# Kernel optimization log

Hardware: AMD Instinct MI355X
Metric: run time of the kernel (lower is better)

The kernel has to match this reference:

```python
import jax, jax.numpy as jnp
import numpy as np

MAX_DET = 300   # max_det in non_max_suppression
IMG = 640       # input image H=W
MH = MW = 160   # proto mask resolution
NM = 32         # mask coefficients
ALPHA = 0.6
MARGIN = 15


def setup_inputs() -> dict:
    key = jax.random.key(0)
    k1, k2, k3, k4, k5, k6 = jax.random.split(key, 6)
    na = 8400
    # realistic YOLOv8 raw head output: xywh in pixels, 1 class score in (0,1), 32 mask coeffs
    cxcy = jax.random.uniform(k1, (1, 2, na), minval=0.0, maxval=float(IMG))
    wh = jax.random.uniform(k2, (1, 2, na), minval=10.0, maxval=200.0)
    cls = jax.random.uniform(k3, (1, 1, na))
    mcoef = jax.random.normal(k4, (1, NM, na))
    prediction = jnp.concatenate([cxcy, wh, cls, mcoef], axis=1)  # [1,37,8400]
    proto = jax.random.normal(k5, (1, NM, MH, MW))
    img = jax.random.uniform(k6, (1, 3, IMG, IMG))
    return {"prediction": prediction, "proto": proto, "img": img,
            "conf_thres": jnp.float32(0.25), "iou_thres": jnp.float32(0.45)}


def _xywh2xyxy(x):
    cx, cy, w, h = x[..., 0], x[..., 1], x[..., 2], x[..., 3]
    return jnp.stack([cx - w / 2, cy - h / 2, cx + w / 2, cy + h / 2], axis=-1)


def _box_iou(b):  # b: [K,4] xyxy -> [K,K] pairwise IoU (torchvision convention)
    x1, y1, x2, y2 = b[:, 0], b[:, 1], b[:, 2], b[:, 3]
    area = (x2 - x1) * (y2 - y1)
    iw = jnp.clip(jnp.minimum(x2[:, None], x2[None, :]) - jnp.maximum(x1[:, None], x1[None, :]), 0)
    ih = jnp.clip(jnp.minimum(y2[:, None], y2[None, :]) - jnp.maximum(y1[:, None], y1[None, :]), 0)
    inter = iw * ih
    return inter / (area[:, None] + area[None, :] - inter + 1e-7)


def _nms_keep(iou, valid, iou_thres):
    # sequential greedy suppression over score-sorted boxes (padded, fixed K)
    K = iou.shape[0]
    def body(keep, i):
        suppressed = jnp.any(keep & (iou[i] > iou_thres))
        keep = keep.at[i].set(valid[i] & ~suppressed)
        return keep, None
    keep, _ = jax.lax.scan(body, jnp.zeros((K,), bool), jnp.arange(K))
    return keep


def reference(prediction, proto, img, conf_thres, iou_thres):
    # --- decode: [1,37,na] -> [na,37], xywh->xyxy (bs=1, nc=1, class offset c = 0*max_wh = 0)
    p = prediction[0].T                      # [na,37]
    boxes = _xywh2xyxy(p[:, :4])             # [na,4]
    conf = p[:, 4]                           # nc=1 -> max over classes is the class itself, j=0
    mcoef = p[:, 5:]                         # [na,32]
    valid = conf > conf_thres
    score = jnp.where(valid, conf, -1.0)
    order = jnp.argsort(-score)[:MAX_DET]    # top max_det candidates by confidence
    boxes_k, score_k, m_k = boxes[order], score[order], mcoef[order]
    valid_k = valid[order]
    # --- NMS (padded)
    keep = _nms_keep(_box_iou(boxes_k), valid_k, iou_thres)  # [K] bool
    # --- process_mask: linear combine protos, sigmoid, crop, bilinear upsample, >0.5
    masks = jax.nn.sigmoid(m_k @ proto[0].reshape(NM, -1)).reshape(MAX_DET, MH, MW)
    scale = jnp.array([MW / IMG, MH / IMG, MW / IMG, MH / IMG], dtype=boxes_k.dtype)
    db = boxes_k * scale                     # downsampled bboxes [K,4]
    r = jnp.arange(MW, dtype=masks.dtype)[None, None, :]
    c = jnp.arange(MH, dtype=masks.dtype)[None, :, None]
    crop = ((r >= db[:, 0, None, None]) & (r < db[:, 2, None, None]) &
            (c >= db[:, 1, None, None]) & (c < db[:, 3, None, None]))
    masks = masks * crop
    masks_up = jax.image.resize(masks, (MAX_DET, IMG, IMG), method='linear')  # align_corners=False bilinear
    masks_bin = (masks_up > 0.5) & keep[:, None, None]       # invalid/suppressed rows zeroed
    # --- scale_boxes: img1_shape == img0_shape -> gain=1, pad=0, just clip
    boxes_c = jnp.clip(boxes_k, 0.0, float(IMG))
    results = jnp.concatenate([boxes_c, score_k[:, None], jnp.zeros((MAX_DET, 1), boxes_c.dtype)], axis=1)
    results = results * keep[:, None].astype(results.dtype)  # [K,6] padded detections
    # --- max-area box -> crop window coords
    areas = jnp.where(keep, (boxes_c[:, 2] - boxes_c[:, 0]) * (boxes_c[:, 3] - boxes_c[:, 1]), 0.0)
    mb = jnp.where(jnp.any(keep), boxes_c[jnp.argmax(areas)], jnp.zeros(4, boxes_c.dtype))
    y1 = jnp.maximum(mb[1].astype(jnp.int32) - MARGIN, 0)
    y2 = jnp.minimum(mb[3].astype(jnp.int32) + MARGIN, IMG)
    x1 = jnp.maximum(mb[0].astype(jnp.int32) - MARGIN, 0)
    x2 = jnp.minimum(mb[2].astype(jnp.int32) + MARGIN, IMG)
    crop_coords = jnp.stack([y1, y2, x1, x2])
    # --- mask overlay blending (stack over images, sum over detections)
    stacked_mk = jnp.sum(masks_bin.astype(img.dtype), axis=0)[None]  # [1,640,640]
    pixels = jnp.count_nonzero(stacked_mk)
    blue = jnp.zeros((3, IMG, IMG), img.dtype).at[2].set(1.0)
    img_out = (1.0 - stacked_mk) * img + stacked_mk * (ALPHA * img + (1.0 - ALPHA) * blue)
    return results, keep, masks_bin, pixels, img_out, crop_coords
```

## Files before the change

### kernel.cpp

```cpp
#include <hip/hip_runtime.h>
#include <stdint.h>

#define NA 8400
#define MAXD 300
#define NMC 32
#define IMGD 640
#define MH 160
#define MW 160
#define PROTO_HW (MH*MW)
#define IMG_HW (IMGD*IMGD)

#define OFF_RESULTS 0
#define OFF_KEEP    1800
#define OFF_MASKS   2100
#define OFF_PIXELS  (2100 + 300*IMG_HW)
#define OFF_IMG     (OFF_PIXELS + 1)
#define OFF_CROP    (OFF_IMG + 3*IMG_HW)

#define WSO_MASKS160 0
#define WSO_KEYS     (MAXD*PROTO_HW*4)
#define WSO_HIST     (WSO_KEYS + NA*8)
#define WSO_META     (WSO_HIST + 1024*4)
#define WSO_ORDER    (WSO_META + 64)
#define WSO_VFLAG    (WSO_ORDER + MAXD*4)
#define WSO_SCORE    (WSO_VFLAG + MAXD*4)
#define WSO_BOXES    (WSO_SCORE + MAXD*4)
#define WSO_MCOEF    (WSO_BOXES + MAXD*16)
#define WSO_KEEPI    (WSO_MCOEF + MAXD*NMC*4)
#define WSO_KLIST    (WSO_KEEPI + MAXD*4)
#define WSO_EBOX     (WSO_KLIST + MAXD*4)

#define NSB 33
#define NFILL 30000

__global__ __launch_bounds__(256)
void k_score_fill(const float* __restrict__ pred, const float* __restrict__ conf_thres_p,
                  uint64_t* __restrict__ keys, unsigned* __restrict__ hist,
                  float* __restrict__ out_masks) {
    int bid = blockIdx.x;
    if (bid >= NSB) {
        size_t f = (size_t)(bid - NSB) * 4096 + (size_t)threadIdx.x * 16;
        float4 z = {0.f, 0.f, 0.f, 0.f};
        float4* p = (float4*)(out_masks + f);
        p[0] = z; p[1] = z; p[2] = z; p[3] = z;
        return;
    }
    int i = bid * 256 + threadIdx.x;
    if (i >= NA) return;
    float th = *conf_thres_p;
    float conf = pred[4 * NA + i];
    uint64_t key = 0;
    if (conf > th) {
        unsigned fb = __float_as_uint(conf);
        key = ((uint64_t)fb << 32) | (unsigned)(NA - 1 - i);
        int bin = (int)(conf * 1024.0f);
        bin = bin < 0 ? 0 : (bin > 1023 ? 1023 : bin);
        atomicAdd(&hist[bin], 1u);
    }
    keys[i] = key;
}

__global__ __launch_bounds__(1024)
void k_select(const float* __restrict__ pred, const uint64_t* __restrict__ keys,
              const unsigned* __restrict__ hist,
              int* __restrict__ vflag, float* __restrict__ score_k,
              float* __restrict__ boxes_k, float* __restrict__ mcoef_k) {
    __shared__ unsigned cum[1024];
    __shared__ uint64_t kl[2048];
    __shared__ uint64_t srt[MAXD];
    __shared__ int s_cnt, s_bcut, s_nsel;
    __shared__ int sorder[MAXD];
    __shared__ int svf[MAXD];
    int t = threadIdx.x;

    cum[t] = hist[t];
    __syncthreads();
    for (int off = 1; off < 1024; off <<= 1) {
        unsigned v = cum[t] + ((t + off < 1024) ? cum[t + off] : 0u);
        __syncthreads();
        cum[t] = v;
        __syncthreads();
    }
    if (t == 0) {
        s_cnt = 0;
        int tot = (int)cum[0];
        s_nsel = tot < MAXD ? tot : MAXD;
        s_bcut = 0;
    }
    __syncthreads();
    int nsel = s_nsel;
    if (nsel > 0) {
        if (cum[t] >= (unsigned)nsel && (t == 1023 || cum[t + 1] < (unsigned)nsel))
            s_bcut = t;
    }
    __syncthreads();
    int bcut = s_bcut;
    if (nsel > 0) {
        for (int i = t; i < NA; i += 1024) {
            uint64_t key = keys[i];
            if (key) {
                float conf = __uint_as_float((unsigned)(key >> 32));
                int bin = (int)(conf * 1024.0f);
                bin = bin > 1023 ? 1023 : bin;
                if (bin >= bcut) {
                    int p = atomicAdd(&s_cnt, 1);
                    if (p < 2048) kl[p] = key;
                }
            }
        }
    }
    __syncthreads();
    int cnt = s_cnt < 2048 ? s_cnt : 2048;
    for (int c = t; c < cnt; c += 1024) {
        uint64_t key = kl[c];
        int rank = 0;
        for (int j = 0; j < cnt; j++) rank += (kl[j] > key) ? 1 : 0;
        if (rank < MAXD) srt[rank] = key;
    }
    __syncthreads();
    if (t < MAXD) {
        int v = (t < nsel) ? 1 : 0;
        uint64_t key = v ? srt[t] : 0;
        int idx = v ? (NA - 1 - (int)(key & 0xffffffffu)) : 0;
        sorder[t] = idx; svf[t] = v;
        vflag[t] = v;
        score_k[t] = v ? __uint_as_float((unsigned)(key >> 32)) : -1.0f;
        float cx = pred[0 * NA + idx], cy = pred[1 * NA + idx];
        float w = pred[2 * NA + idx], h = pred[3 * NA + idx];
        float b0 = cx - w * 0.5f, b1 = cy - h * 0.5f, b2 = cx + w * 0.5f, b3 = cy + h * 0.5f;
        if (!v) { b0 = b1 = b2 = b3 = 0.f; }
        boxes_k[t * 4 + 0] = b0; boxes_k[t * 4 + 1] = b1;
        boxes_k[t * 4 + 2] = b2; boxes_k[t * 4 + 3] = b3;
    }
    __syncthreads();
    for (int m = t; m < MAXD * NMC; m += 1024) {
        int r = m >> 5, c = m & 31;
        mcoef_k[m] = svf[r] ? pred[(5 + c) * NA + sorder[r]] : 0.f;
    }
}

__global__ __launch_bounds__(512)
void k_nms(const float* __restrict__ iou_thres_p, const int* __restrict__ vflag,
           const float* __restrict__ boxes_k, const float* __restrict__ score_k,
           int* __restrict__ keepi, int* __restrict__ klist, int* __restrict__ meta,
           int* __restrict__ ebox, float* __restrict__ out) {
    __shared__ uint64_t su[MAXD][5];
    __shared__ float bx[MAXD][4];
    __shared__ float sarea[MAXD];
    __shared__ int sv[MAXD];
    __shared__ int skeep[MAXD];
    int t = threadIdx.x;
    for (int i = t; i < MAXD; i += 512) {
        float b0 = boxes_k[i * 4 + 0], b1 = boxes_k[i * 4 + 1];
        float b2 = boxes_k[i * 4 + 2], b3 = boxes_k[i * 4 + 3];
        bx[i][0] = b0; bx[i][1] = b1; bx[i][2] = b2; bx[i][3] = b3;
        sarea[i] = (b2 - b0) * (b3 - b1);
        sv[i] = vflag[i];
    }
    __syncthreads();
    float ithr = *iou_thres_p;
    if (t < MAXD) {
        float x1 = bx[t][0], y1 = bx[t][1], x2 = bx[t][2], y2 = bx[t][3];
        float ar = sarea[t];
        uint64_t m[5] = {0, 0, 0, 0, 0};
        for (int j = 0; j < MAXD; j++) {
            float iw = fmaxf(fminf(x2, bx[j][2]) - fmaxf(x1, bx[j][0]), 0.f);
            float ih = fmaxf(fminf(y2, bx[j][3]) - fmaxf(y1, bx[j][1]), 0.f);
            float inter = iw * ih;
            float iou = inter / (ar + sarea[j] - inter + 1e-7f);
            if (iou > ithr) m[j >> 6] |= 1ull << (j & 63);
        }
        for (int w = 0; w < 5; w++) su[t][w] = m[w];

        float db0 = x1 * 0.25f, db1 = y1 * 0.25f, db2 = x2 * 0.25f, db3 = y2 * 0.25f;
        int pxmin = max(0, (int)ceilf(db0));
        int pxmax = min(MW - 1, (int)ceilf(db2) - 1);
        int pymin = max(0, (int)ceilf(db1));
        int pymax = min(MH - 1, (int)ceilf(db3) - 1);
        int xlo = 1, xhi = 0, ylo = 1, yhi = 0;
        if (pxmin <= pxmax && pymin <= pymax) {
            xlo = max(0, 4 * pxmin - 2); xhi = min(IMGD - 1, 4 * pxmax + 5);
            ylo = max(0, 4 * pymin - 2); yhi = min(IMGD - 1, 4 * pymax + 5);
        }
        ebox[t * 4 + 0] = xlo; ebox[t * 4 + 1] = xhi;
        ebox[t * 4 + 2] = ylo; ebox[t * 4 + 3] = yhi;
    }
    __syncthreads();
    if (t < 64) {
        uint64_t kwl = 0;
        int lane = t;
        for (int i = 0; i < MAXD; i++) {
            uint64_t x = (lane < 5) ? (su[i][lane] & kwl) : 0;
            bool sup = __any(x != 0);
            bool k = sv[i] && !sup;
            if (lane == (i >> 6) && k) kwl |= 1ull << (i & 63);
            if (lane == 0) { skeep[i] = k ? 1 : 0; keepi[i] = k ? 1 : 0; }
        }
    }
    __syncthreads();
    if (t < MAXD) {
        bool k = skeep[t] != 0;
        float bc0 = fminf(fmaxf(bx[t][0], 0.f), 640.f);
        float bc1 = fminf(fmaxf(bx[t][1], 0.f), 640.f);
        float bc2 = fminf(fmaxf(bx[t][2], 0.f), 640.f);
        float bc3 = fminf(fmaxf(bx[t][3], 0.f), 640.f);
        out[OFF_RESULTS + t * 6 + 0] = k ? bc0 : 0.f;
        out[OFF_RESULTS + t * 6 + 1] = k ? bc1 : 0.f;
        out[OFF_RESULTS + t * 6 + 2] = k ? bc2 : 0.f;
        out[OFF_RESULTS + t * 6 + 3] = k ? bc3 : 0.f;
        out[OFF_RESULTS + t * 6 + 4] = k ? score_k[t] : 0.f;
        out[OFF_RESULTS + t * 6 + 5] = 0.f;
        out[OFF_KEEP + t] = k ? 1.f : 0.f;
    }
    if (t == 0) {
        int n = 0;
        bool anyk = false;
        for (int i = 0; i < MAXD; i++)
            if (skeep[i]) { klist[n++] = i; anyk = true; }
        meta[0] = n;
        float amax = -INFINITY; int ai = 0;
        for (int i = 0; i < MAXD; i++) {
            float bc0 = fminf(fmaxf(bx[i][0], 0.f), 640.f);
            float bc1 = fminf(fmaxf(bx[i][1], 0.f), 640.f);
            float bc2 = fminf(fmaxf(bx[i][2], 0.f), 640.f);
            float bc3 = fminf(fmaxf(bx[i][3], 0.f), 640.f);
            float a = skeep[i] ? (bc2 - bc0) * (bc3 - bc1) : 0.f;
            if (a > amax) { amax = a; ai = i; }
        }
        float mb0 = 0.f, mb1 = 0.f, mb2 = 0.f, mb3 = 0.f;
        if (anyk) {
            mb0 = fminf(fmaxf(bx[ai][0], 0.f), 640.f);
            mb1 = fminf(fmaxf(bx[ai][1], 0.f), 640.f);
            mb2 = fminf(fmaxf(bx[ai][2], 0.f), 640.f);
            mb3 = fminf(fmaxf(bx[ai][3], 0.f), 640.f);
        }
        int y1 = max((int)mb1 - 15, 0);
        int y2 = min((int)mb3 + 15, IMGD);
        int x1 = max((int)mb0 - 15, 0);
        int x2 = min((int)mb2 + 15, IMGD);
        out[OFF_CROP + 0] = (float)y1;
        out[OFF_CROP + 1] = (float)y2;
        out[OFF_CROP + 2] = (float)x1;
        out[OFF_CROP + 3] = (float)x2;
    }
}

__global__ __launch_bounds__(256)
void k_masks(const float* __restrict__ proto, const float* __restrict__ mcoef_k,
             const float* __restrict__ boxes_k, const int* __restrict__ keepi,
             float* __restrict__ masks160) {
    int slot = blockIdx.y;
    if (!keepi[slot]) return;
    __shared__ float co[NMC];
    __shared__ float db[4];
    int t = threadIdx.x;
    if (t < NMC) co[t] = mcoef_k[slot * NMC + t];
    if (t >= NMC && t < NMC + 4) db[t - NMC] = boxes_k[slot * 4 + (t - NMC)] * 0.25f;
    __syncthreads();
    int p = blockIdx.x * 256 + t;
    float acc = 0.f;
#pragma unroll
    for (int k = 0; k < NMC; k++) acc = fmaf(co[k], proto[k * PROTO_HW + p], acc);
    float sig = 1.f / (1.f + expf(-acc));
    int py = p / MW, px = p - py * MW;
    float r = (float)px, c = (float)py;
    bool crop = (r >= db[0]) && (r < db[2]) && (c >= db[1]) && (c < db[3]);
    masks160[slot * PROTO_HW + p] = crop ? sig : 0.f;
}

__device__ __forceinline__ float bilin(const float* __restrict__ m, int y, int x) {
    float sy = 0.25f * (float)y - 0.375f;
    float sx = 0.25f * (float)x - 0.375f;
    int y0 = (int)floorf(sy); float fy = sy - (float)y0;
    int x0 = (int)floorf(sx); float fx = sx - (float)x0;
    if (y0 < 0) { y0 = 0; fy = 0.f; }
    int y1 = y0 + 1; if (y1 > MH - 1) { y1 = MH - 1; fy = 0.f; }
    if (x0 < 0) { x0 = 0; fx = 0.f; }
    int x1 = x0 + 1; if (x1 > MW - 1) { x1 = MW - 1; fx = 0.f; }
    const float* r0 = m + y0 * MW;
    const float* r1 = m + y1 * MW;
    float v00 = r0[x0], v01 = r0[x1], v10 = r1[x0], v11 = r1[x1];
    float t0 = fmaf(fy, v10, (1.f - fy) * v00);
    float t1 = fmaf(fy, v11, (1.f - fy) * v01);
    return fmaf(fx, t1, (1.f - fx) * t0);
}

__global__ __launch_bounds__(256)
void k_paint(const float* __restrict__ masks160, const int* __restrict__ keepi,
             const int* __restrict__ ebox, float* __restrict__ out_masks) {
    int det = blockIdx.y;
    if (!keepi[det]) return;
    int xlo = ebox[det * 4 + 0], xhi = ebox[det * 4 + 1];
    int ylo = ebox[det * 4 + 2], yhi = ebox[det * 4 + 3];
    if (xlo > xhi || ylo > yhi) return;
    int xlo0 = xlo & ~3;
    int q = blockIdx.x * 256 + threadIdx.x;
    int rx = q % 56, ry = q / 56;
    const float* m = masks160 + (size_t)det * PROTO_HW;
    float* od = out_masks + (size_t)det * IMG_HW;
    for (int y = ylo + ry; y <= yhi; y += 224) {
        for (int x = xlo0 + 4 * rx; x <= xhi; x += 224) {
            float4 o;
            o.x = (bilin(m, y, x)     > 0.5f) ? 1.f : 0.f;
            o.y = (bilin(m, y, x + 1) > 0.5f) ? 1.f : 0.f;
            o.z = (bilin(m, y, x + 2) > 0.5f) ? 1.f : 0.f;
            o.w = (bilin(m, y, x + 3) > 0.5f) ? 1.f : 0.f;
            *(float4*)(od + y * IMGD + x) = o;
        }
    }
}

__global__ __launch_bounds__(256)
void k_blend(const float* __restrict__ masks160, const int* __restrict__ klist,
             const int* __restrict__ ebox, const int* __restrict__ meta,
             const float* __restrict__ img, float* __restrict__ out,
             int* __restrict__ pix_count) {
    __shared__ int sxlo[MAXD], sxhi[MAXD], sylo[MAXD], syhi[MAXD], soff[MAXD];
    int n = meta[0];
    int t = threadIdx.x;
    for (int i = t; i < n; i += 256) {
        int d = klist[i];
        sxlo[i] = ebox[d * 4 + 0]; sxhi[i] = ebox[d * 4 + 1];
        sylo[i] = ebox[d * 4 + 2]; syhi[i] = ebox[d * 4 + 3];
        soff[i] = d * PROTO_HW;
    }
    __syncthreads();
    int base = (blockIdx.x * 256 + t) * 4;
    int y = base / IMGD, x = base - y * IMGD;
    float4 s = {0.f, 0.f, 0.f, 0.f};
    for (int i = 0; i < n; i++) {
        if (y >= sylo[i] && y <= syhi[i] && x + 3 >= sxlo[i] && x <= sxhi[i]) {
            const float* m = masks160 + soff[i];
            s.x += (bilin(m, y, x)     > 0.5f) ? 1.f : 0.f;
            s.y += (bilin(m, y, x + 1) > 0.5f) ? 1.f : 0.f;
            s.z += (bilin(m, y, x + 2) > 0.5f) ? 1.f : 0.f;
            s.w += (bilin(m, y, x + 3) > 0.5f) ? 1.f : 0.f;
        }
    }
#pragma unroll
    for (int c = 0; c < 3; c++) {
        float4 iv = *(const float4*)(img + c * IMG_HW + base);
        float bl = (c == 2) ? 1.f : 0.f;
        float4 ov;
        ov.x = (1.f - s.x) * iv.x + s.x * (0.6f * iv.x + 0.4f * bl);
        ov.y = (1.f - s.y) * iv.y + s.y * (0.6f * iv.y + 0.4f * bl);
        ov.z = (1.f - s.z) * iv.z + s.z * (0.6f * iv.z + 0.4f * bl);
        ov.w = (1.f - s.w) * iv.w + s.w * (0.6f * iv.w + 0.4f * bl);
        *(float4*)(out + OFF_IMG + c * IMG_HW + base) = ov;
    }
    int cnt = (s.x != 0.f) + (s.y != 0.f) + (s.z != 0.f) + (s.w != 0.f);
    for (int o2 = 32; o2 > 0; o2 >>= 1) cnt += __shfl_down(cnt, o2, 64);
    if ((t & 63) == 0) atomicAdd(pix_count, cnt);
}

__global__ void k_final(const int* __restrict__ meta, float* __restrict__ out) {
    out[OFF_PIXELS] = (float)meta[1];
}

extern "C" void kernel_launch(void* const* d_in, const int* in_sizes, int n_in,
                              void* d_out, int out_size, void* d_ws, size_t ws_size,
                              hipStream_t stream) {
    const float* pred       = (const float*)d_in[0];
    const float* proto      = (const float*)d_in[1];
    const float* img        = (const float*)d_in[2];
    const float* conf_thres = (const float*)d_in[3];
    const float* iou_thres  = (const float*)d_in[4];
    float* out = (float*)d_out;
    char* ws = (char*)d_ws;

    float*    masks160 = (float*)(ws + WSO_MASKS160);
    uint64_t* keys     = (uint64_t*)(ws + WSO_KEYS);
    unsigned* hist     = (unsigned*)(ws + WSO_HIST);
    int*      meta     = (int*)(ws + WSO_META);
    int*      vflag    = (int*)(ws + WSO_VFLAG);
    float*    score_k  = (float*)(ws + WSO_SCORE);
    float*    boxes_k  = (float*)(ws + WSO_BOXES);
    float*    mcoef_k  = (float*)(ws + WSO_MCOEF);
    int*      keepi    = (int*)(ws + WSO_KEEPI);
    int*      klist    = (int*)(ws + WSO_KLIST);
    int*      ebox     = (int*)(ws + WSO_EBOX);

    hipMemsetAsync(ws + WSO_HIST, 0, 1024 * 4 + 64, stream);

    k_score_fill<<<dim3(NSB + NFILL), dim3(256), 0, stream>>>(pred, conf_thres, keys, hist,
                                                              out + OFF_MASKS);
    k_select<<<dim3(1), dim3(1024), 0, stream>>>(pred, keys, hist, vflag, score_k, boxes_k, mcoef_k);
    k_nms<<<dim3(1), dim3(512), 0, stream>>>(iou_thres, vflag, boxes_k, score_k, keepi, klist, meta, ebox, out);
    k_masks<<<dim3(PROTO_HW / 256, MAXD), dim3(256), 0, stream>>>(proto, mcoef_k, boxes_k, keepi, masks160);
    k_paint<<<dim3(49, MAXD), dim3(256), 0, stream>>>(masks160, keepi, ebox, out + OFF_MASKS);
    k_blend<<<dim3(IMG_HW / 1024), dim3(256), 0, stream>>>(masks160, klist, ebox, meta, img, out, meta + 1);
    k_final<<<dim3(1), dim3(1), 0, stream>>>(meta, out);
}
```

Measured before the change: 811.9 us.

## Fuse select with NMS and mask zero-fill with upsample and blend

```diff
diff --git a/kernel.cpp b/kernel.cpp
--- a/kernel.cpp
+++ b/kernel.cpp
@@ -18,62 +18,43 @@
 #define OFF_CROP    (OFF_IMG + 3*IMG_HW)
 
 #define WSO_MASKS160 0
-#define WSO_KEYS     (MAXD*PROTO_HW*4)
-#define WSO_HIST     (WSO_KEYS + NA*8)
-#define WSO_META     (WSO_HIST + 1024*4)
-#define WSO_ORDER    (WSO_META + 64)
-#define WSO_VFLAG    (WSO_ORDER + MAXD*4)
-#define WSO_SCORE    (WSO_VFLAG + MAXD*4)
-#define WSO_BOXES    (WSO_SCORE + MAXD*4)
+#define WSO_META     (MAXD*PROTO_HW*4)
+#define WSO_BOXES    (WSO_META + 64)
 #define WSO_MCOEF    (WSO_BOXES + MAXD*16)
 #define WSO_KEEPI    (WSO_MCOEF + MAXD*NMC*4)
 #define WSO_KLIST    (WSO_KEEPI + MAXD*4)
 #define WSO_EBOX     (WSO_KLIST + MAXD*4)
 
-#define NSB 33
-#define NFILL 30000
-
-__global__ __launch_bounds__(256)
-void k_score_fill(const float* __restrict__ pred, const float* __restrict__ conf_thres_p,
-                  uint64_t* __restrict__ keys, unsigned* __restrict__ hist,
-                  float* __restrict__ out_masks) {
-    int bid = blockIdx.x;
-    if (bid >= NSB) {
-        size_t f = (size_t)(bid - NSB) * 4096 + (size_t)threadIdx.x * 16;
-        float4 z = {0.f, 0.f, 0.f, 0.f};
-        float4* p = (float4*)(out_masks + f);
-        p[0] = z; p[1] = z; p[2] = z; p[3] = z;
-        return;
-    }
-    int i = bid * 256 + threadIdx.x;
-    if (i >= NA) return;
-    float th = *conf_thres_p;
-    float conf = pred[4 * NA + i];
-    uint64_t key = 0;
-    if (conf > th) {
-        unsigned fb = __float_as_uint(conf);
-        key = ((uint64_t)fb << 32) | (unsigned)(NA - 1 - i);
-        int bin = (int)(conf * 1024.0f);
-        bin = bin < 0 ? 0 : (bin > 1023 ? 1023 : bin);
-        atomicAdd(&hist[bin], 1u);
-    }
-    keys[i] = key;
-}
-
 __global__ __launch_bounds__(1024)
-void k_select(const float* __restrict__ pred, const uint64_t* __restrict__ keys,
-              const unsigned* __restrict__ hist,
-              int* __restrict__ vflag, float* __restrict__ score_k,
-              float* __restrict__ boxes_k, float* __restrict__ mcoef_k) {
+void k_selnms(const float* __restrict__ pred, const float* __restrict__ conf_thres_p,
+              const float* __restrict__ iou_thres_p,
+              int* __restrict__ keepi, int* __restrict__ klist, int* __restrict__ meta,
+              int* __restrict__ ebox, float* __restrict__ boxes_k,
+              float* __restrict__ mcoef_k, float* __restrict__ out) {
     __shared__ unsigned cum[1024];
     __shared__ uint64_t kl[2048];
     __shared__ uint64_t srt[MAXD];
     __shared__ int s_cnt, s_bcut, s_nsel;
     __shared__ int sorder[MAXD];
     __shared__ int svf[MAXD];
+    __shared__ float sscore[MAXD];
+    __shared__ float bx[MAXD][4];
+    __shared__ float sarea[MAXD];
+    __shared__ uint64_t su[MAXD][5];
+    __shared__ int skeep[MAXD];
     int t = threadIdx.x;
-
-    cum[t] = hist[t];
+    float th = *conf_thres_p;
+
+    cum[t] = 0;
+    __syncthreads();
+    for (int i = t; i < NA; i += 1024) {
+        float conf = pred[4 * NA + i];
+        if (conf > th) {
+            int bin = (int)(conf * 1024.0f);
+            bin = bin < 0 ? 0 : (bin > 1023 ? 1023 : bin);
+            atomicAdd(&cum[bin], 1u);
+        }
+    }
     __syncthreads();
     for (int off = 1; off < 1024; off <<= 1) {
         unsigned v = cum[t] + ((t + off < 1024) ? cum[t + off] : 0u);
@@ -97,14 +78,16 @@
     int bcut = s_bcut;
     if (nsel > 0) {
         for (int i = t; i < NA; i += 1024) {
-            uint64_t key = keys[i];
-            if (key) {
-                float conf = __uint_as_float((unsigned)(key >> 32));
+            float conf = pred[4 * NA + i];
+            if (conf > th) {
                 int bin = (int)(conf * 1024.0f);
-                bin = bin > 1023 ? 1023 : bin;
+                bin = bin < 0 ? 0 : (bin > 1023 ? 1023 : bin);
                 if (bin >= bcut) {
                     int p = atomicAdd(&s_cnt, 1);
-                    if (p < 2048) kl[p] = key;
+                    if (p < 2048) {
+                        unsigned fb = __float_as_uint(conf);
+                        kl[p] = ((uint64_t)fb << 32) | (unsigned)(NA - 1 - i);
+                    }
                 }
             }
         }
@@ -123,12 +106,13 @@
         uint64_t key = v ? srt[t] : 0;
         int idx = v ? (NA - 1 - (int)(key & 0xffffffffu)) : 0;
         sorder[t] = idx; svf[t] = v;
-        vflag[t] = v;
-        score_k[t] = v ? __uint_as_float((unsigned)(key >> 32)) : -1.0f;
+        sscore[t] = v ? __uint_as_float((unsigned)(key >> 32)) : -1.0f;
         float cx = pred[0 * NA + idx], cy = pred[1 * NA + idx];
         float w = pred[2 * NA + idx], h = pred[3 * NA + idx];
         float b0 = cx - w * 0.5f, b1 = cy - h * 0.5f, b2 = cx + w * 0.5f, b3 = cy + h * 0.5f;
         if (!v) { b0 = b1 = b2 = b3 = 0.f; }
+        bx[t][0] = b0; bx[t][1] = b1; bx[t][2] = b2; bx[t][3] = b3;
+        sarea[t] = (b2 - b0) * (b3 - b1);
         boxes_k[t * 4 + 0] = b0; boxes_k[t * 4 + 1] = b1;
         boxes_k[t * 4 + 2] = b2; boxes_k[t * 4 + 3] = b3;
     }
@@ -137,27 +121,6 @@
         int r = m >> 5, c = m & 31;
         mcoef_k[m] = svf[r] ? pred[(5 + c) * NA + sorder[r]] : 0.f;
     }
-}
-
-__global__ __launch_bounds__(512)
-void k_nms(const float* __restrict__ iou_thres_p, const int* __restrict__ vflag,
-           const float* __restrict__ boxes_k, const float* __restrict__ score_k,
-           int* __restrict__ keepi, int* __restrict__ klist, int* __restrict__ meta,
-           int* __restrict__ ebox, float* __restrict__ out) {
-    __shared__ uint64_t su[MAXD][5];
-    __shared__ float bx[MAXD][4];
-    __shared__ float sarea[MAXD];
-    __shared__ int sv[MAXD];
-    __shared__ int skeep[MAXD];
-    int t = threadIdx.x;
-    for (int i = t; i < MAXD; i += 512) {
-        float b0 = boxes_k[i * 4 + 0], b1 = boxes_k[i * 4 + 1];
-        float b2 = boxes_k[i * 4 + 2], b3 = boxes_k[i * 4 + 3];
-        bx[i][0] = b0; bx[i][1] = b1; bx[i][2] = b2; bx[i][3] = b3;
-        sarea[i] = (b2 - b0) * (b3 - b1);
-        sv[i] = vflag[i];
-    }
-    __syncthreads();
     float ithr = *iou_thres_p;
     if (t < MAXD) {
         float x1 = bx[t][0], y1 = bx[t][1], x2 = bx[t][2], y2 = bx[t][3];
@@ -171,7 +134,6 @@
             if (iou > ithr) m[j >> 6] |= 1ull << (j & 63);
         }
         for (int w = 0; w < 5; w++) su[t][w] = m[w];
-
         float db0 = x1 * 0.25f, db1 = y1 * 0.25f, db2 = x2 * 0.25f, db3 = y2 * 0.25f;
         int pxmin = max(0, (int)ceilf(db0));
         int pxmax = min(MW - 1, (int)ceilf(db2) - 1);
@@ -192,7 +154,7 @@
         for (int i = 0; i < MAXD; i++) {
             uint64_t x = (lane < 5) ? (su[i][lane] & kwl) : 0;
             bool sup = __any(x != 0);
-            bool k = sv[i] && !sup;
+            bool k = svf[i] && !sup;
             if (lane == (i >> 6) && k) kwl |= 1ull << (i & 63);
             if (lane == 0) { skeep[i] = k ? 1 : 0; keepi[i] = k ? 1 : 0; }
         }
@@ -208,7 +170,7 @@
         out[OFF_RESULTS + t * 6 + 1] = k ? bc1 : 0.f;
         out[OFF_RESULTS + t * 6 + 2] = k ? bc2 : 0.f;
         out[OFF_RESULTS + t * 6 + 3] = k ? bc3 : 0.f;
-        out[OFF_RESULTS + t * 6 + 4] = k ? score_k[t] : 0.f;
+        out[OFF_RESULTS + t * 6 + 4] = k ? sscore[t] : 0.f;
         out[OFF_RESULTS + t * 6 + 5] = 0.f;
         out[OFF_KEEP + t] = k ? 1.f : 0.f;
     }
@@ -218,6 +180,7 @@
         for (int i = 0; i < MAXD; i++)
             if (skeep[i]) { klist[n++] = i; anyk = true; }
         meta[0] = n;
+        meta[1] = 0;
         float amax = -INFINITY; int ai = 0;
         for (int i = 0; i < MAXD; i++) {
             float bc0 = fminf(fmaxf(bx[i][0], 0.f), 640.f);
@@ -286,38 +249,43 @@
 }
 
 __global__ __launch_bounds__(256)
-void k_paint(const float* __restrict__ masks160, const int* __restrict__ keepi,
-             const int* __restrict__ ebox, float* __restrict__ out_masks) {
+void k_upblend(const float* __restrict__ masks160, const int* __restrict__ keepi,
+               const int* __restrict__ klist, const int* __restrict__ ebox,
+               const int* __restrict__ meta, const float* __restrict__ img,
+               float* __restrict__ out, int* __restrict__ pix_count) {
     int det = blockIdx.y;
-    if (!keepi[det]) return;
-    int xlo = ebox[det * 4 + 0], xhi = ebox[det * 4 + 1];
-    int ylo = ebox[det * 4 + 2], yhi = ebox[det * 4 + 3];
-    if (xlo > xhi || ylo > yhi) return;
-    int xlo0 = xlo & ~3;
-    int q = blockIdx.x * 256 + threadIdx.x;
-    int rx = q % 56, ry = q / 56;
-    const float* m = masks160 + (size_t)det * PROTO_HW;
-    float* od = out_masks + (size_t)det * IMG_HW;
-    for (int y = ylo + ry; y <= yhi; y += 224) {
-        for (int x = xlo0 + 4 * rx; x <= xhi; x += 224) {
-            float4 o;
-            o.x = (bilin(m, y, x)     > 0.5f) ? 1.f : 0.f;
-            o.y = (bilin(m, y, x + 1) > 0.5f) ? 1.f : 0.f;
-            o.z = (bilin(m, y, x + 2) > 0.5f) ? 1.f : 0.f;
-            o.w = (bilin(m, y, x + 3) > 0.5f) ? 1.f : 0.f;
-            *(float4*)(od + y * IMGD + x) = o;
-        }
-    }
-}
-
-__global__ __launch_bounds__(256)
-void k_blend(const float* __restrict__ masks160, const int* __restrict__ klist,
-             const int* __restrict__ ebox, const int* __restrict__ meta,
-             const float* __restrict__ img, float* __restrict__ out,
-             int* __restrict__ pix_count) {
+    int t = threadIdx.x;
+    int seg = (blockIdx.x * 256 + t) * 16;
+    int y = seg / IMGD, x16 = seg - y * IMGD;
+
+    if (det < MAXD) {
+        float4* dst = (float4*)(out + OFF_MASKS + (size_t)det * IMG_HW + seg);
+        float4 z = {0.f, 0.f, 0.f, 0.f};
+        bool inside = false;
+        if (keepi[det]) {
+            int xlo = ebox[det * 4 + 0], xhi = ebox[det * 4 + 1];
+            int ylo = ebox[det * 4 + 2], yhi = ebox[det * 4 + 3];
+            inside = (y >= ylo && y <= yhi && x16 + 15 >= xlo && x16 <= xhi);
+        }
+        if (!inside) {
+            dst[0] = z; dst[1] = z; dst[2] = z; dst[3] = z;
+            return;
+        }
+        const float* m = masks160 + (size_t)det * PROTO_HW;
+        float v[16];
+#pragma unroll
+        for (int j = 0; j < 16; j++)
+            v[j] = (bilin(m, y, x16 + j) > 0.5f) ? 1.f : 0.f;
+#pragma unroll
+        for (int q = 0; q < 4; q++) {
+            float4 o = {v[4 * q], v[4 * q + 1], v[4 * q + 2], v[4 * q + 3]};
+            dst[q] = o;
+        }
+        return;
+    }
+
     __shared__ int sxlo[MAXD], sxhi[MAXD], sylo[MAXD], syhi[MAXD], soff[MAXD];
     int n = meta[0];
-    int t = threadIdx.x;
     for (int i = t; i < n; i += 256) {
         int d = klist[i];
         sxlo[i] = ebox[d * 4 + 0]; sxhi[i] = ebox[d * 4 + 1];
@@ -325,30 +293,37 @@
         soff[i] = d * PROTO_HW;
     }
     __syncthreads();
-    int base = (blockIdx.x * 256 + t) * 4;
-    int y = base / IMGD, x = base - y * IMGD;
-    float4 s = {0.f, 0.f, 0.f, 0.f};
+    float s[16];
+#pragma unroll
+    for (int j = 0; j < 16; j++) s[j] = 0.f;
     for (int i = 0; i < n; i++) {
-        if (y >= sylo[i] && y <= syhi[i] && x + 3 >= sxlo[i] && x <= sxhi[i]) {
+        if (y >= sylo[i] && y <= syhi[i] && x16 + 15 >= sxlo[i] && x16 <= sxhi[i]) {
             const float* m = masks160 + soff[i];
-            s.x += (bilin(m, y, x)     > 0.5f) ? 1.f : 0.f;
-            s.y += (bilin(m, y, x + 1) > 0.5f) ? 1.f : 0.f;
-            s.z += (bilin(m, y, x + 2) > 0.5f) ? 1.f : 0.f;
-            s.w += (bilin(m, y, x + 3) > 0.5f) ? 1.f : 0.f;
+#pragma unroll
+            for (int j = 0; j < 16; j++)
+                s[j] += (bilin(m, y, x16 + j) > 0.5f) ? 1.f : 0.f;
         }
     }
 #pragma unroll
     for (int c = 0; c < 3; c++) {
-        float4 iv = *(const float4*)(img + c * IMG_HW + base);
+        const float4* iv = (const float4*)(img + (size_t)c * IMG_HW + seg);
+        float4* ov = (float4*)(out + OFF_IMG + (size_t)c * IMG_HW + seg);
         float bl = (c == 2) ? 1.f : 0.f;
-        float4 ov;
-        ov.x = (1.f - s.x) * iv.x + s.x * (0.6f * iv.x + 0.4f * bl);
-        ov.y = (1.f - s.y) * iv.y + s.y * (0.6f * iv.y + 0.4f * bl);
-        ov.z = (1.f - s.z) * iv.z + s.z * (0.6f * iv.z + 0.4f * bl);
-        ov.w = (1.f - s.w) * iv.w + s.w * (0.6f * iv.w + 0.4f * bl);
-        *(float4*)(out + OFF_IMG + c * IMG_HW + base) = ov;
-    }
-    int cnt = (s.x != 0.f) + (s.y != 0.f) + (s.z != 0.f) + (s.w != 0.f);
+#pragma unroll
+        for (int q = 0; q < 4; q++) {
+            float4 inq = iv[q];
+            float4 o;
+            float sv0 = s[4 * q], sv1 = s[4 * q + 1], sv2 = s[4 * q + 2], sv3 = s[4 * q + 3];
+            o.x = (1.f - sv0) * inq.x + sv0 * (0.6f * inq.x + 0.4f * bl);
+            o.y = (1.f - sv1) * inq.y + sv1 * (0.6f * inq.y + 0.4f * bl);
+            o.z = (1.f - sv2) * inq.z + sv2 * (0.6f * inq.z + 0.4f * bl);
+            o.w = (1.f - sv3) * inq.w + sv3 * (0.6f * inq.w + 0.4f * bl);
+            ov[q] = o;
+        }
+    }
+    int cnt = 0;
+#pragma unroll
+    for (int j = 0; j < 16; j++) cnt += (s[j] != 0.f) ? 1 : 0;
     for (int o2 = 32; o2 > 0; o2 >>= 1) cnt += __shfl_down(cnt, o2, 64);
     if ((t & 63) == 0) atomicAdd(pix_count, cnt);
 }
@@ -368,26 +343,18 @@
     float* out = (float*)d_out;
     char* ws = (char*)d_ws;
 
-    float*    masks160 = (float*)(ws + WSO_MASKS160);
-    uint64_t* keys     = (uint64_t*)(ws + WSO_KEYS);
-    unsigned* hist     = (unsigned*)(ws + WSO_HIST);
-    int*      meta     = (int*)(ws + WSO_META);
-    int*      vflag    = (int*)(ws + WSO_VFLAG);
-    float*    score_k  = (float*)(ws + WSO_SCORE);
-    float*    boxes_k  = (float*)(ws + WSO_BOXES);
-    float*    mcoef_k  = (float*)(ws + WSO_MCOEF);
-    int*      keepi    = (int*)(ws + WSO_KEEPI);
-    int*      klist    = (int*)(ws + WSO_KLIST);
-    int*      ebox     = (int*)(ws + WSO_EBOX);
-
-    hipMemsetAsync(ws + WSO_HIST, 0, 1024 * 4 + 64, stream);
-
-    k_score_fill<<<dim3(NSB + NFILL), dim3(256), 0, stream>>>(pred, conf_thres, keys, hist,
-                                                              out + OFF_MASKS);
-    k_select<<<dim3(1), dim3(1024), 0, stream>>>(pred, keys, hist, vflag, score_k, boxes_k, mcoef_k);
-    k_nms<<<dim3(1), dim3(512), 0, stream>>>(iou_thres, vflag, boxes_k, score_k, keepi, klist, meta, ebox, out);
+    float* masks160 = (float*)(ws + WSO_MASKS160);
+    int*   meta     = (int*)(ws + WSO_META);
+    float* boxes_k  = (float*)(ws + WSO_BOXES);
+    float* mcoef_k  = (float*)(ws + WSO_MCOEF);
+    int*   keepi    = (int*)(ws + WSO_KEEPI);
+    int*   klist    = (int*)(ws + WSO_KLIST);
+    int*   ebox     = (int*)(ws + WSO_EBOX);
+
+    k_selnms<<<dim3(1), dim3(1024), 0, stream>>>(pred, conf_thres, iou_thres,
+                                                 keepi, klist, meta, ebox, boxes_k, mcoef_k, out);
     k_masks<<<dim3(PROTO_HW / 256, MAXD), dim3(256), 0, stream>>>(proto, mcoef_k, boxes_k, keepi, masks160);
-    k_paint<<<dim3(49, MAXD), dim3(256), 0, stream>>>(masks160, keepi, ebox, out + OFF_MASKS);
-    k_blend<<<dim3(IMG_HW / 1024), dim3(256), 0, stream>>>(masks160, klist, ebox, meta, img, out, meta + 1);
+    k_upblend<<<dim3(IMG_HW / 4096, MAXD + 1), dim3(256), 0, stream>>>(masks160, keepi, klist, ebox,
+                                                                       meta, img, out, meta + 1);
     k_final<<<dim3(1), dim3(1), 0, stream>>>(meta, out);
 }
```

Measured after the change: 833.5 us. 1.03x slower.
